# Performance work log

Measured on AMD Instinct MI355X. Metric: run time of the kernel, lower is better.

The kernel has to match this reference:

```python
import jax, jax.numpy as jnp
import numpy as np

N_POINTS = 262144
L_LEVELS = 16
FEATS_PER_LEVEL = 2
BASE_RES = 8
FINEST_RES = 512
TABLE_SIZE = 2 ** 12  # log2_hashmap_size = 12
HIDDEN = 256
IN_FEATURES = 3
MLP_IN = L_LEVELS * FEATS_PER_LEVEL + IN_FEATURES - 2  # 33


def _level_params():
    b = np.exp((np.log(FINEST_RES) - np.log(BASE_RES)) / (L_LEVELS - 1))
    res = np.floor(BASE_RES * b ** np.arange(L_LEVELS)).astype(np.int64)
    hsize = np.minimum(res ** 2, TABLE_SIZE)  # per-level hashmap size
    return jnp.asarray(res, jnp.float32), jnp.asarray(hsize, jnp.uint32)


RES, HSIZE = _level_params()
PRIMES = jnp.array([1, 2654435761], dtype=jnp.uint32)  # instant-NGP spatial hash primes (2D)
CORNERS = jnp.array([[0, 0], [0, 1], [1, 0], [1, 1]], dtype=jnp.int32)  # [4,2]


def hash_encode(coords, tables):
    # coords: [N,2] in [0,1]; tables: [L, TABLE_SIZE, F]
    x = coords[None, :, :] * RES[:, None, None]            # [L,N,2] scaled per level
    xi = jnp.floor(x)
    xf = x - xi                                            # fractional part (grad flows to coords)
    inds = xi.astype(jnp.int32)[:, :, None, :] + CORNERS   # [L,N,4,2] corner integer coords
    # bilinear weights: offset 0 -> (1-xf), offset 1 -> xf
    w = jnp.prod(jnp.where(CORNERS == 0, 1.0 - xf[:, :, None, :], xf[:, :, None, :]), axis=-1)  # [L,N,4]
    u = inds.astype(jnp.uint32) * PRIMES                   # [L,N,4,2]
    h = (u[..., 0] ^ u[..., 1]) % HSIZE[:, None, None]     # [L,N,4] hashed table index
    feats = jax.vmap(lambda t, i: t[i])(tables, h)         # [L,N,4,F] gather per level
    out = jnp.einsum('lncf,lnc->lnf', feats, w)            # [L,N,F] bilinear interp
    return jnp.moveaxis(out, 0, 1).reshape(coords.shape[0], -1)  # [N, L*F], level-major per point


def reference(x, tables, W0, b0, W1, b1, W2, b2, W3, b3, W4, b4):
    h = hash_encode(x[:, :2], tables)                      # [N, 32]
    h = jnp.concatenate([h, x[:, 2:]], axis=-1)            # [N, 33]
    h = jax.nn.relu(h @ W0 + b0)
    h = jax.nn.relu(h @ W1 + b1)
    h = jax.nn.relu(h @ W2 + b2)
    h = jax.nn.relu(h @ W3 + b3)
    return h @ W4 + b4                                     # [N, 1]


def setup_inputs() -> dict:
    key = jax.random.key(0)
    ks = jax.random.split(key, 12)

    def lin(kw, fan_in, fan_out):
        s = 1.0 / np.sqrt(fan_in)
        return jax.random.normal(kw, (fan_in, fan_out), jnp.float32) * s

    return {
        'x': jax.random.uniform(ks[0], (N_POINTS, IN_FEATURES), jnp.float32),
        'tables': jax.random.normal(ks[1], (L_LEVELS, TABLE_SIZE, FEATS_PER_LEVEL), jnp.float32) * 1e-2,
        'W0': lin(ks[2], MLP_IN, HIDDEN), 'b0': jnp.zeros((HIDDEN,), jnp.float32),
        'W1': lin(ks[3], HIDDEN, HIDDEN), 'b1': jnp.zeros((HIDDEN,), jnp.float32),
        'W2': lin(ks[4], HIDDEN, HIDDEN), 'b2': jnp.zeros((HIDDEN,), jnp.float32),
        'W3': lin(ks[5], HIDDEN, HIDDEN), 'b3': jnp.zeros((HIDDEN,), jnp.float32),
        'W4': lin(ks[6], HIDDEN, 1),      'b4': jnp.zeros((1,), jnp.float32),
    }
```

## Files before the change

### kernel.cpp

```cpp
#include <hip/hip_runtime.h>
#include <math.h>


typedef __bf16 bf16x8 __attribute__((ext_vector_type(8)));
typedef float  f32x4  __attribute__((ext_vector_type(4)));
typedef unsigned int u32x4 __attribute__((ext_vector_type(4)));

struct LevelParams { float res[16]; unsigned int hsize[16]; };

static constexpr int MTILE = 128;
static constexpr int LDA   = 264;
static constexpr int ACT_ELEMS = MTILE * LDA;
static constexpr int UNITS_L0 = 32;
static constexpr int UB_L0 = 0, UB_L1 = 32, UB_L2 = 160, UB_L3 = 288;
static constexpr int UNITS_TOTAL = 416;

__device__ __forceinline__ unsigned short f32_to_bf16_rne(float f) {
  unsigned u = __float_as_uint(f);
  unsigned r = (u + 0x7fffu + ((u >> 16) & 1u)) >> 16;
  return (unsigned short)r;
}
__device__ __forceinline__ float bf16_bits_to_f32(unsigned short h) {
  return __uint_as_float(((unsigned)h) << 16);
}
__device__ __forceinline__ void split_store(unsigned short* ahi, unsigned short* alo,
                                            int idx, float v) {
  unsigned short h = f32_to_bf16_rne(v);
  float hf = bf16_bits_to_f32(h);
  unsigned short lo = f32_to_bf16_rne(v - hf);
  ahi[idx] = h;
  alo[idx] = lo;
}

__global__ void prep_pack(const float* __restrict__ W0, const float* __restrict__ W1,
                          const float* __restrict__ W2, const float* __restrict__ W3,
                          unsigned short* __restrict__ pack) {
  int b = blockIdx.x;
  int lane = threadIdx.x;
  const float* W; int K; int r;
  if (b < UNITS_L0) { W = W0; K = 33; r = b; }
  else {
    int b2 = b - UNITS_L0; int ly = b2 >> 7; r = b2 & 127;
    W = (ly == 0) ? W1 : (ly == 1) ? W2 : W3; K = 256;
  }
  int s = r >> 4, ct = r & 15;
  int col   = (ct << 4) + (lane & 15);
  int kbase = (s << 5) + ((lane >> 4) << 3);
  unsigned short* dst = pack + (size_t)b * 1024;
#pragma unroll
  for (int e = 0; e < 8; ++e) {
    int k = kbase + e;
    float v = (k < K) ? W[k * 256 + col] : 0.0f;
    unsigned short h = f32_to_bf16_rne(v);
    float hf = bf16_bits_to_f32(h);
    unsigned short lo = f32_to_bf16_rne(v - hf);
    dst[lane * 8 + e]       = h;
    dst[512 + lane * 8 + e] = lo;
  }
}

__device__ __forceinline__ void run_layer(unsigned short* ahi, unsigned short* alo,
                                          const unsigned short* __restrict__ pack,
                                          int unitbase, int S,
                                          const float* __restrict__ bias,
                                          int wr, int wc, int lm, int lg, int lane) {
  f32x4 acc[4][4];
#pragma unroll
  for (int i = 0; i < 4; ++i)
#pragma unroll
    for (int j = 0; j < 4; ++j) acc[i][j] = (f32x4)0.0f;

  for (int s = 0; s < S; ++s) {
    bf16x8 a_h[4], a_l[4], b_h[4], b_l[4];
#pragma unroll
    for (int rt = 0; rt < 4; ++rt) {
      int row = (wr << 6) + (rt << 4) + lm;
      int off = row * LDA + (s << 5) + (lg << 3);
      u32x4 th = *(const u32x4*)(ahi + off);
      u32x4 tl = *(const u32x4*)(alo + off);
      a_h[rt] = __builtin_bit_cast(bf16x8, th);
      a_l[rt] = __builtin_bit_cast(bf16x8, tl);
    }
#pragma unroll
    for (int ct = 0; ct < 4; ++ct) {
      int unit = unitbase + (s << 4) + (wc << 2) + ct;
      const unsigned short* bp = pack + (size_t)unit * 1024 + (lane << 3);
      u32x4 th = *(const u32x4*)(bp);
      u32x4 tl = *(const u32x4*)(bp + 512);
      b_h[ct] = __builtin_bit_cast(bf16x8, th);
      b_l[ct] = __builtin_bit_cast(bf16x8, tl);
    }
#pragma unroll
    for (int rt = 0; rt < 4; ++rt)
#pragma unroll
      for (int ct = 0; ct < 4; ++ct) {
        acc[rt][ct] = __builtin_amdgcn_mfma_f32_16x16x32_bf16(a_h[rt], b_h[ct], acc[rt][ct], 0, 0, 0);
        acc[rt][ct] = __builtin_amdgcn_mfma_f32_16x16x32_bf16(a_l[rt], b_h[ct], acc[rt][ct], 0, 0, 0);
        acc[rt][ct] = __builtin_amdgcn_mfma_f32_16x16x32_bf16(a_h[rt], b_l[ct], acc[rt][ct], 0, 0, 0);
      }
  }
  __syncthreads();
#pragma unroll
  for (int ct = 0; ct < 4; ++ct) {
    int col = (((wc << 2) + ct) << 4) + lm;
    float bv = bias[col];
#pragma unroll
    for (int rt = 0; rt < 4; ++rt) {
#pragma unroll
      for (int r = 0; r < 4; ++r) {
        int row = (wr << 6) + (rt << 4) + (lg << 2) + r;
        float v = acc[rt][ct][r] + bv;
        v = fmaxf(v, 0.0f);
        split_store(ahi, alo, row * LDA + col, v);
      }
    }
  }
  __syncthreads();
}

__global__ __launch_bounds__(512, 1) void inr_main(
    const float* __restrict__ x, const float* __restrict__ tables,
    const float* __restrict__ b0, const float* __restrict__ b1,
    const float* __restrict__ b2, const float* __restrict__ b3,
    const float* __restrict__ W4, const float* __restrict__ b4,
    const unsigned short* __restrict__ pack, float* __restrict__ out,
    LevelParams P) {
  extern __shared__ char smem[];
  unsigned short* ahi = (unsigned short*)smem;
  unsigned short* alo = ahi + ACT_ELEMS;
  float* w4s = (float*)(alo + ACT_ELEMS);

  const int tid = threadIdx.x;
  if (tid < 256) w4s[tid] = W4[tid];

  {
    int pl = tid >> 2, q = tid & 3;
    size_t p = (size_t)blockIdx.x * MTILE + pl;
    float x0 = x[3 * p + 0], x1 = x[3 * p + 1], x2 = x[3 * p + 2];
#pragma unroll
    for (int j = 0; j < 4; ++j) {
      int l = (q << 2) + j;
      float rf = P.res[l];
      unsigned hs = P.hsize[l];
      float xs0 = x0 * rf, xs1 = x1 * rf;
      float fl0 = floorf(xs0), fl1 = floorf(xs1);
      float f0 = xs0 - fl0, f1 = xs1 - fl1;
      int i0 = (int)fl0, i1 = (int)fl1;
      unsigned ua0 = (unsigned)i0, ua1 = (unsigned)(i0 + 1);
      unsigned vb0 = (unsigned)i1 * 2654435761u;
      unsigned vb1 = (unsigned)(i1 + 1) * 2654435761u;
      const float* tl = tables + ((size_t)l << 13);
      float g0 = 1.0f - f0, g1 = 1.0f - f1;
      float acc0 = 0.0f, acc1 = 0.0f;
      { unsigned h = (ua0 ^ vb0) % hs; float w = g0 * g1; acc0 += w * tl[2*h]; acc1 += w * tl[2*h+1]; }
      { unsigned h = (ua0 ^ vb1) % hs; float w = g0 * f1; acc0 += w * tl[2*h]; acc1 += w * tl[2*h+1]; }
      { unsigned h = (ua1 ^ vb0) % hs; float w = f0 * g1; acc0 += w * tl[2*h]; acc1 += w * tl[2*h+1]; }
      { unsigned h = (ua1 ^ vb1) % hs; float w = f0 * f1; acc0 += w * tl[2*h]; acc1 += w * tl[2*h+1]; }
      int base = pl * LDA + (l << 1);
      split_store(ahi, alo, base, acc0);
      split_store(ahi, alo, base + 1, acc1);
    }
    int cb = 32 + (q << 3);
#pragma unroll
    for (int e = 0; e < 8; ++e) {
      int col = cb + e;
      float v = (col == 32) ? x2 : 0.0f;
      split_store(ahi, alo, pl * LDA + col, v);
    }
  }
  __syncthreads();

  const int lane = tid & 63;
  const int w = tid >> 6;
  const int wr = w >> 2, wc = w & 3;
  const int lm = lane & 15, lg = lane >> 4;

  run_layer(ahi, alo, pack, UB_L0, 2, b0, wr, wc, lm, lg, lane);
  run_layer(ahi, alo, pack, UB_L1, 8, b1, wr, wc, lm, lg, lane);
  run_layer(ahi, alo, pack, UB_L2, 8, b2, wr, wc, lm, lg, lane);
  run_layer(ahi, alo, pack, UB_L3, 8, b3, wr, wc, lm, lg, lane);

  {
    int pl = tid >> 2, q = tid & 3;
    const unsigned short* hrow = ahi + pl * LDA + (q << 6);
    const unsigned short* lrow = alo + pl * LDA + (q << 6);
    const float* w4p = w4s + (q << 6);
    float sum = 0.0f;
#pragma unroll
    for (int k = 0; k < 64; ++k) {
      float v = bf16_bits_to_f32(hrow[k]) + bf16_bits_to_f32(lrow[k]);
      sum = fmaf(v, w4p[k], sum);
    }
    sum += __shfl_xor(sum, 1);
    sum += __shfl_xor(sum, 2);
    if (q == 0) out[(size_t)blockIdx.x * MTILE + pl] = sum + b4[0];
  }
}

extern "C" void kernel_launch(void* const* d_in, const int* in_sizes, int n_in,
                              void* d_out, int out_size, void* d_ws, size_t ws_size,
                              hipStream_t stream) {
  const float* x      = (const float*)d_in[0];
  const float* tables = (const float*)d_in[1];
  const float* W0 = (const float*)d_in[2];  const float* b0 = (const float*)d_in[3];
  const float* W1 = (const float*)d_in[4];  const float* b1 = (const float*)d_in[5];
  const float* W2 = (const float*)d_in[6];  const float* b2 = (const float*)d_in[7];
  const float* W3 = (const float*)d_in[8];  const float* b3 = (const float*)d_in[9];
  const float* W4 = (const float*)d_in[10]; const float* b4 = (const float*)d_in[11];
  unsigned short* pack = (unsigned short*)d_ws;
  float* out = (float*)d_out;

  LevelParams P;
  double bgrow = exp((log(512.0) - log(8.0)) / 15.0);
  for (int l = 0; l < 16; ++l) {
    double r = floor(8.0 * pow(bgrow, (double)l));
    P.res[l] = (float)r;
    double hsd = r * r;
    if (hsd > 4096.0) hsd = 4096.0;
    P.hsize[l] = (unsigned)hsd;
  }

  prep_pack<<<UNITS_TOTAL, 64, 0, stream>>>(W0, W1, W2, W3, pack);

  size_t smem_bytes = (size_t)ACT_ELEMS * 2 * 2 + 256 * sizeof(float);
  hipFuncSetAttribute(reinterpret_cast<const void*>(inr_main),
                      hipFuncAttributeMaxDynamicSharedMemorySize, (int)smem_bytes);

  int nblocks = out_size / MTILE;
  inr_main<<<nblocks, 512, smem_bytes, stream>>>(x, tables, b0, b1, b2, b3, W4, b4,
                                                 pack, out, P);
}
```

Before: 307.4 us.

## Shrink tile to 64 points, swap MFMA operands, vectorize LDS stores, raise occupancy

Halves the point tile to 64 rows so that all 8 waves split columns, and lifts the launch bound to 4 blocks per CU so more blocks can be resident. MFMA operands are swapped so the weights act as the A operand and each lane's accumulator holds 4 consecutive columns. That lets the epilogue write the hi/lo bf16 split with packed 64-bit LDS stores. It also truncates the hi part instead of rounding it, takes a fast mask path for power-of-two hash sizes, and reads W4 straight from global memory. Together this targets LDS store overhead and latency hiding, at the cost of re-reading weights twice as often per point.

```diff
diff --git a/kernel.cpp b/kernel.cpp
--- a/kernel.cpp
+++ b/kernel.cpp
@@ -5,10 +5,11 @@
 typedef __bf16 bf16x8 __attribute__((ext_vector_type(8)));
 typedef float  f32x4  __attribute__((ext_vector_type(4)));
 typedef unsigned int u32x4 __attribute__((ext_vector_type(4)));
+typedef unsigned int u32x2 __attribute__((ext_vector_type(2)));
 
 struct LevelParams { float res[16]; unsigned int hsize[16]; };
 
-static constexpr int MTILE = 128;
+static constexpr int MTILE = 64;
 static constexpr int LDA   = 264;
 static constexpr int ACT_ELEMS = MTILE * LDA;
 static constexpr int UNITS_L0 = 32;
@@ -20,16 +21,8 @@
   unsigned r = (u + 0x7fffu + ((u >> 16) & 1u)) >> 16;
   return (unsigned short)r;
 }
-__device__ __forceinline__ float bf16_bits_to_f32(unsigned short h) {
-  return __uint_as_float(((unsigned)h) << 16);
-}
-__device__ __forceinline__ void split_store(unsigned short* ahi, unsigned short* alo,
-                                            int idx, float v) {
-  unsigned short h = f32_to_bf16_rne(v);
-  float hf = bf16_bits_to_f32(h);
-  unsigned short lo = f32_to_bf16_rne(v - hf);
-  ahi[idx] = h;
-  alo[idx] = lo;
+__device__ __forceinline__ float bf16_bits_to_f32(unsigned u16bits) {
+  return __uint_as_float(u16bits << 16);
 }
 
 __global__ void prep_pack(const float* __restrict__ W0, const float* __restrict__ W1,
@@ -51,8 +44,9 @@
   for (int e = 0; e < 8; ++e) {
     int k = kbase + e;
     float v = (k < K) ? W[k * 256 + col] : 0.0f;
-    unsigned short h = f32_to_bf16_rne(v);
-    float hf = bf16_bits_to_f32(h);
+    unsigned u = __float_as_uint(v);
+    unsigned short h = (unsigned short)(u >> 16);
+    float hf = bf16_bits_to_f32(u >> 16);
     unsigned short lo = f32_to_bf16_rne(v - hf);
     dst[lane * 8 + e]       = h;
     dst[512 + lane * 8 + e] = lo;
@@ -63,62 +57,66 @@
                                           const unsigned short* __restrict__ pack,
                                           int unitbase, int S,
                                           const float* __restrict__ bias,
-                                          int wr, int wc, int lm, int lg, int lane) {
-  f32x4 acc[4][4];
+                                          int wc, int lm, int lg, int lane) {
+  f32x4 acc[4][2];
 #pragma unroll
   for (int i = 0; i < 4; ++i)
 #pragma unroll
-    for (int j = 0; j < 4; ++j) acc[i][j] = (f32x4)0.0f;
+    for (int j = 0; j < 2; ++j) acc[i][j] = (f32x4)0.0f;
 
   for (int s = 0; s < S; ++s) {
-    bf16x8 a_h[4], a_l[4], b_h[4], b_l[4];
-#pragma unroll
-    for (int rt = 0; rt < 4; ++rt) {
-      int row = (wr << 6) + (rt << 4) + lm;
-      int off = row * LDA + (s << 5) + (lg << 3);
-      u32x4 th = *(const u32x4*)(ahi + off);
-      u32x4 tl = *(const u32x4*)(alo + off);
-      a_h[rt] = __builtin_bit_cast(bf16x8, th);
-      a_l[rt] = __builtin_bit_cast(bf16x8, tl);
-    }
-#pragma unroll
-    for (int ct = 0; ct < 4; ++ct) {
-      int unit = unitbase + (s << 4) + (wc << 2) + ct;
+    bf16x8 w_h[2], w_l[2], a_h[4], a_l[4];
+#pragma unroll
+    for (int ct = 0; ct < 2; ++ct) {
+      int unit = unitbase + (s << 4) + (wc << 1) + ct;
       const unsigned short* bp = pack + (size_t)unit * 1024 + (lane << 3);
-      u32x4 th = *(const u32x4*)(bp);
-      u32x4 tl = *(const u32x4*)(bp + 512);
-      b_h[ct] = __builtin_bit_cast(bf16x8, th);
-      b_l[ct] = __builtin_bit_cast(bf16x8, tl);
-    }
-#pragma unroll
-    for (int rt = 0; rt < 4; ++rt)
-#pragma unroll
-      for (int ct = 0; ct < 4; ++ct) {
-        acc[rt][ct] = __builtin_amdgcn_mfma_f32_16x16x32_bf16(a_h[rt], b_h[ct], acc[rt][ct], 0, 0, 0);
-        acc[rt][ct] = __builtin_amdgcn_mfma_f32_16x16x32_bf16(a_l[rt], b_h[ct], acc[rt][ct], 0, 0, 0);
-        acc[rt][ct] = __builtin_amdgcn_mfma_f32_16x16x32_bf16(a_h[rt], b_l[ct], acc[rt][ct], 0, 0, 0);
+      w_h[ct] = __builtin_bit_cast(bf16x8, *(const u32x4*)(bp));
+      w_l[ct] = __builtin_bit_cast(bf16x8, *(const u32x4*)(bp + 512));
+    }
+#pragma unroll
+    for (int pt = 0; pt < 4; ++pt) {
+      int off = ((pt << 4) + lm) * LDA + (s << 5) + (lg << 3);
+      a_h[pt] = __builtin_bit_cast(bf16x8, *(const u32x4*)(ahi + off));
+      a_l[pt] = __builtin_bit_cast(bf16x8, *(const u32x4*)(alo + off));
+    }
+#pragma unroll
+    for (int pt = 0; pt < 4; ++pt)
+#pragma unroll
+      for (int ct = 0; ct < 2; ++ct) {
+        acc[pt][ct] = __builtin_amdgcn_mfma_f32_16x16x32_bf16(w_h[ct], a_h[pt], acc[pt][ct], 0, 0, 0);
+        acc[pt][ct] = __builtin_amdgcn_mfma_f32_16x16x32_bf16(w_l[ct], a_h[pt], acc[pt][ct], 0, 0, 0);
+        acc[pt][ct] = __builtin_amdgcn_mfma_f32_16x16x32_bf16(w_h[ct], a_l[pt], acc[pt][ct], 0, 0, 0);
       }
   }
   __syncthreads();
 #pragma unroll
-  for (int ct = 0; ct < 4; ++ct) {
-    int col = (((wc << 2) + ct) << 4) + lm;
-    float bv = bias[col];
-#pragma unroll
-    for (int rt = 0; rt < 4; ++rt) {
-#pragma unroll
-      for (int r = 0; r < 4; ++r) {
-        int row = (wr << 6) + (rt << 4) + (lg << 2) + r;
-        float v = acc[rt][ct][r] + bv;
-        v = fmaxf(v, 0.0f);
-        split_store(ahi, alo, row * LDA + col, v);
-      }
-    }
-  }
+  for (int pt = 0; pt < 4; ++pt)
+#pragma unroll
+    for (int ct = 0; ct < 2; ++ct) {
+      int colbase = (((wc << 1) + ct) << 4) + (lg << 2);
+      float4 bv = *(const float4*)(bias + colbase);
+      int base = ((pt << 4) + lm) * LDA + colbase;
+      float v0 = fmaxf(acc[pt][ct][0] + bv.x, 0.0f);
+      float v1 = fmaxf(acc[pt][ct][1] + bv.y, 0.0f);
+      float v2 = fmaxf(acc[pt][ct][2] + bv.z, 0.0f);
+      float v3 = fmaxf(acc[pt][ct][3] + bv.w, 0.0f);
+      unsigned u0 = __float_as_uint(v0), u1 = __float_as_uint(v1);
+      unsigned u2 = __float_as_uint(v2), u3 = __float_as_uint(v3);
+      u32x2 hw = { (u0 >> 16) | (u1 & 0xffff0000u),
+                   (u2 >> 16) | (u3 & 0xffff0000u) };
+      float l0 = v0 - bf16_bits_to_f32(u0 >> 16);
+      float l1 = v1 - bf16_bits_to_f32(u1 >> 16);
+      float l2 = v2 - bf16_bits_to_f32(u2 >> 16);
+      float l3 = v3 - bf16_bits_to_f32(u3 >> 16);
+      u32x2 lw = { (unsigned)f32_to_bf16_rne(l0) | ((unsigned)f32_to_bf16_rne(l1) << 16),
+                   (unsigned)f32_to_bf16_rne(l2) | ((unsigned)f32_to_bf16_rne(l3) << 16) };
+      *(u32x2*)(ahi + base) = hw;
+      *(u32x2*)(alo + base) = lw;
+    }
   __syncthreads();
 }
 
-__global__ __launch_bounds__(512, 1) void inr_main(
+__global__ __launch_bounds__(512, 4) void inr_main(
     const float* __restrict__ x, const float* __restrict__ tables,
     const float* __restrict__ b0, const float* __restrict__ b1,
     const float* __restrict__ b2, const float* __restrict__ b3,
@@ -128,18 +126,17 @@
   extern __shared__ char smem[];
   unsigned short* ahi = (unsigned short*)smem;
   unsigned short* alo = ahi + ACT_ELEMS;
-  float* w4s = (float*)(alo + ACT_ELEMS);
 
   const int tid = threadIdx.x;
-  if (tid < 256) w4s[tid] = W4[tid];
 
   {
-    int pl = tid >> 2, q = tid & 3;
+    int pl = tid >> 3, q = tid & 7;
     size_t p = (size_t)blockIdx.x * MTILE + pl;
     float x0 = x[3 * p + 0], x1 = x[3 * p + 1], x2 = x[3 * p + 2];
-#pragma unroll
-    for (int j = 0; j < 4; ++j) {
-      int l = (q << 2) + j;
+    float feat[4];
+#pragma unroll
+    for (int j = 0; j < 2; ++j) {
+      int l = (q << 1) + j;
       float rf = P.res[l];
       unsigned hs = P.hsize[l];
       float xs0 = x0 * rf, xs1 = x1 * rf;
@@ -152,47 +149,87 @@
       const float* tl = tables + ((size_t)l << 13);
       float g0 = 1.0f - f0, g1 = 1.0f - f1;
       float acc0 = 0.0f, acc1 = 0.0f;
-      { unsigned h = (ua0 ^ vb0) % hs; float w = g0 * g1; acc0 += w * tl[2*h]; acc1 += w * tl[2*h+1]; }
-      { unsigned h = (ua0 ^ vb1) % hs; float w = g0 * f1; acc0 += w * tl[2*h]; acc1 += w * tl[2*h+1]; }
-      { unsigned h = (ua1 ^ vb0) % hs; float w = f0 * g1; acc0 += w * tl[2*h]; acc1 += w * tl[2*h+1]; }
-      { unsigned h = (ua1 ^ vb1) % hs; float w = f0 * f1; acc0 += w * tl[2*h]; acc1 += w * tl[2*h+1]; }
-      int base = pl * LDA + (l << 1);
-      split_store(ahi, alo, base, acc0);
-      split_store(ahi, alo, base + 1, acc1);
-    }
-    int cb = 32 + (q << 3);
-#pragma unroll
-    for (int e = 0; e < 8; ++e) {
-      int col = cb + e;
-      float v = (col == 32) ? x2 : 0.0f;
-      split_store(ahi, alo, pl * LDA + col, v);
+      unsigned e0 = ua0 ^ vb0, e1 = ua0 ^ vb1, e2 = ua1 ^ vb0, e3 = ua1 ^ vb1;
+      unsigned h0, h1, h2, h3;
+      if (hs == 4096u) { h0 = e0 & 4095u; h1 = e1 & 4095u; h2 = e2 & 4095u; h3 = e3 & 4095u; }
+      else             { h0 = e0 % hs;    h1 = e1 % hs;    h2 = e2 % hs;    h3 = e3 % hs; }
+      { float w = g0 * g1; acc0 += w * tl[2*h0]; acc1 += w * tl[2*h0+1]; }
+      { float w = g0 * f1; acc0 += w * tl[2*h1]; acc1 += w * tl[2*h1+1]; }
+      { float w = f0 * g1; acc0 += w * tl[2*h2]; acc1 += w * tl[2*h2+1]; }
+      { float w = f0 * f1; acc0 += w * tl[2*h3]; acc1 += w * tl[2*h3+1]; }
+      feat[2*j] = acc0; feat[2*j+1] = acc1;
+    }
+    {
+      int base = pl * LDA + (q << 2);
+      unsigned u0 = __float_as_uint(feat[0]), u1 = __float_as_uint(feat[1]);
+      unsigned u2 = __float_as_uint(feat[2]), u3 = __float_as_uint(feat[3]);
+      u32x2 hw = { (u0 >> 16) | (u1 & 0xffff0000u), (u2 >> 16) | (u3 & 0xffff0000u) };
+      float l0 = feat[0] - bf16_bits_to_f32(u0 >> 16);
+      float l1 = feat[1] - bf16_bits_to_f32(u1 >> 16);
+      float l2 = feat[2] - bf16_bits_to_f32(u2 >> 16);
+      float l3 = feat[3] - bf16_bits_to_f32(u3 >> 16);
+      u32x2 lw = { (unsigned)f32_to_bf16_rne(l0) | ((unsigned)f32_to_bf16_rne(l1) << 16),
+                   (unsigned)f32_to_bf16_rne(l2) | ((unsigned)f32_to_bf16_rne(l3) << 16) };
+      *(u32x2*)(ahi + base) = hw;
+      *(u32x2*)(alo + base) = lw;
+    }
+    {
+      int base = pl * LDA + 32 + (q << 2);
+      if (q == 0) {
+        unsigned u0 = __float_as_uint(x2);
+        u32x2 hw = { u0 >> 16, 0u };
+        float l0 = x2 - bf16_bits_to_f32(u0 >> 16);
+        u32x2 lw = { (unsigned)f32_to_bf16_rne(l0), 0u };
+        *(u32x2*)(ahi + base) = hw;
+        *(u32x2*)(alo + base) = lw;
+      } else {
+        u32x2 z = { 0u, 0u };
+        *(u32x2*)(ahi + base) = z;
+        *(u32x2*)(alo + base) = z;
+      }
     }
   }
   __syncthreads();
 
   const int lane = tid & 63;
-  const int w = tid >> 6;
-  const int wr = w >> 2, wc = w & 3;
+  const int wc = tid >> 6;
   const int lm = lane & 15, lg = lane >> 4;
 
-  run_layer(ahi, alo, pack, UB_L0, 2, b0, wr, wc, lm, lg, lane);
-  run_layer(ahi, alo, pack, UB_L1, 8, b1, wr, wc, lm, lg, lane);
-  run_layer(ahi, alo, pack, UB_L2, 8, b2, wr, wc, lm, lg, lane);
-  run_layer(ahi, alo, pack, UB_L3, 8, b3, wr, wc, lm, lg, lane);
+  run_layer(ahi, alo, pack, UB_L0, 2, b0, wc, lm, lg, lane);
+  run_layer(ahi, alo, pack, UB_L1, 8, b1, wc, lm, lg, lane);
+  run_layer(ahi, alo, pack, UB_L2, 8, b2, wc, lm, lg, lane);
+  run_layer(ahi, alo, pack, UB_L3, 8, b3, wc, lm, lg, lane);
 
   {
-    int pl = tid >> 2, q = tid & 3;
-    const unsigned short* hrow = ahi + pl * LDA + (q << 6);
-    const unsigned short* lrow = alo + pl * LDA + (q << 6);
-    const float* w4p = w4s + (q << 6);
+    int pl = tid >> 3, q = tid & 7;
+    const unsigned short* hrow = ahi + pl * LDA + (q << 5);
+    const unsigned short* lrow = alo + pl * LDA + (q << 5);
+    const float* w4p = W4 + (q << 5);
     float sum = 0.0f;
 #pragma unroll
-    for (int k = 0; k < 64; ++k) {
-      float v = bf16_bits_to_f32(hrow[k]) + bf16_bits_to_f32(lrow[k]);
-      sum = fmaf(v, w4p[k], sum);
+    for (int c = 0; c < 4; ++c) {
+      u32x4 th = *(const u32x4*)(hrow + (c << 3));
+      u32x4 tl = *(const u32x4*)(lrow + (c << 3));
+      float4 wA = *(const float4*)(w4p + (c << 3));
+      float4 wB = *(const float4*)(w4p + (c << 3) + 4);
+#pragma unroll
+      for (int e = 0; e < 4; ++e) {
+        unsigned hu = th[e >> 1], lu = tl[e >> 1];
+        unsigned sh = (e & 1) << 4;
+        float v = bf16_bits_to_f32((hu >> sh) & 0xffffu) + bf16_bits_to_f32((lu >> sh) & 0xffffu);
+        sum = fmaf(v, (&wA.x)[e], sum);
+      }
+#pragma unroll
+      for (int e = 0; e < 4; ++e) {
+        unsigned hu = th[2 + (e >> 1)], lu = tl[2 + (e >> 1)];
+        unsigned sh = (e & 1) << 4;
+        float v = bf16_bits_to_f32((hu >> sh) & 0xffffu) + bf16_bits_to_f32((lu >> sh) & 0xffffu);
+        sum = fmaf(v, (&wB.x)[e], sum);
+      }
     }
     sum += __shfl_xor(sum, 1);
     sum += __shfl_xor(sum, 2);
+    sum += __shfl_xor(sum, 4);
     if (q == 0) out[(size_t)blockIdx.x * MTILE + pl] = sum + b4[0];
   }
 }
@@ -222,7 +259,7 @@
 
   prep_pack<<<UNITS_TOTAL, 64, 0, stream>>>(W0, W1, W2, W3, pack);
 
-  size_t smem_bytes = (size_t)ACT_ELEMS * 2 * 2 + 256 * sizeof(float);
+  size_t smem_bytes = (size_t)ACT_ELEMS * 2 * 2;
   hipFuncSetAttribute(reinterpret_cast<const void*>(inr_main),
                       hipFuncAttributeMaxDynamicSharedMemorySize, (int)smem_bytes);
 
```

Result: faster. 288.2 us (-6.2%).
